# Performance work log

Measured on AMD Instinct MI355X. Metric: run time of the kernel, lower is better.

The kernel has to match this reference:

```python
import jax, jax.numpy as jnp
import numpy as np

B, N, D, H = 256, 40, 256, 256      # molecules, atoms/molecule, pc_hidden, pred_hidden
nS, nC, nB = 40, 5, 5               # n_SYMBOLS, n_FORMAL_CHARGES, n_BOND_TYPES
NEG_SLOPE = 0.01                    # F.leaky_relu default


def _lrelu(x):
    return jnp.where(x >= 0, x, NEG_SLOPE * x)


def setup_inputs() -> dict:
    key = jax.random.key(0)
    ks = jax.random.split(key, 7)
    def w(k, shape, fan_in):
        return jax.random.normal(k, shape, jnp.float32) / np.float32(np.sqrt(fan_in))
    return {
        "yhat": jax.random.normal(ks[0], (B, N, D), jnp.float32),
        "Ws1": w(ks[1], (D, H), D),      "bs1": jnp.zeros((H,), jnp.float32),
        "Ws2": w(ks[2], (H, nS), H),     "bs2": jnp.zeros((nS,), jnp.float32),
        "Wc1": w(ks[3], (D, H), D),      "bc1": jnp.zeros((H,), jnp.float32),
        "Wc2": w(ks[4], (H, nC), H),     "bc2": jnp.zeros((nC,), jnp.float32),
        "Wb1": w(ks[5], (2 * D, H), 2 * D), "bb1": jnp.zeros((H,), jnp.float32),
        "Wb2": w(ks[6], (H, nB), H),     "bb2": jnp.zeros((nB,), jnp.float32),
    }


def reference(yhat, Ws1, bs1, Ws2, bs2, Wc1, bc1, Wc2, bc2, Wb1, bb1, Wb2, bb2):
    # Per-atom symbol / charge heads (2-layer MLP with leaky_relu)
    symbols = _lrelu(yhat @ Ws1 + bs1) @ Ws2 + bs2          # [B, N, nS]
    charges = _lrelu(yhat @ Wc1 + bc1) @ Wc2 + bc2          # [B, N, nC]

    # Pairwise bond head: concat(x_i, x_j) @ Wb1 == x_i @ Wb1[:D] + x_j @ Wb1[D:]
    # (avoids materializing the [B, N, N, 2D] concat tensor)
    p1 = yhat @ Wb1[:D]                                      # [B, N, H]
    p2 = yhat @ Wb1[D:]                                      # [B, N, H]
    h = _lrelu(p1[:, :, None, :] + p2[:, None, :, :] + bb1)  # [B, N, N, H]
    bonds = h @ Wb2 + bb2                                    # [B, N, N, nB]
    bonds = bonds + jnp.swapaxes(bonds, 1, 2)                # symmetrize (i,j)+(j,i)

    return (symbols.reshape(-1, nS),
            charges.reshape(-1, nC),
            bonds.reshape(-1, nB))
```

## Files before the change

kernel.cpp:

```cpp
#include <hip/hip_runtime.h>
#include <hip/hip_bf16.h>

typedef unsigned short u16;
typedef __attribute__((ext_vector_type(4))) int   int4v;
typedef __attribute__((ext_vector_type(4))) unsigned int uint4v;
typedef __attribute__((ext_vector_type(4))) unsigned short ushort4v;
typedef __attribute__((ext_vector_type(4))) float floatx4;
typedef __attribute__((ext_vector_type(8))) short bf16x8;

#define LRELU_NS 0.01f
#define SK 264

__device__ __forceinline__ float bitsToF(unsigned int b) {
    union { unsigned int u; float f; } v; v.u = b << 16; return v.f;
}
__device__ __forceinline__ float bfLo(unsigned int d) {
    union { unsigned int u; float f; } v; v.u = d << 16; return v.f;
}
__device__ __forceinline__ float bfHi(unsigned int d) {
    union { unsigned int u; float f; } v; v.u = d & 0xffff0000u; return v.f;
}
__device__ __forceinline__ u16 f2bf(float f) {
    __hip_bfloat16 h = __float2bfloat16(f);
    return *reinterpret_cast<u16*>(&h);
}
__device__ __forceinline__ float lrelu(float v) {
    return fmaxf(v, 0.f) + LRELU_NS * fminf(v, 0.f);
}
__device__ __forceinline__ u16 ldW(const void* p, int i, int isF32) {
    return isF32 ? f2bf(((const float*)p)[i]) : ((const u16*)p)[i];
}
__device__ __forceinline__ float ldF(const void* p, int i, int isF32) {
    return isF32 ? ((const float*)p)[i]
                 : bitsToF((unsigned int)((const u16*)p)[i]);
}

__device__ __forceinline__ int computeIsF32(const u16* y, int* cnt, int t) {
    if (t == 0) *cnt = 0;
    __syncthreads();
    if (t < 256) {
        u16 v = y[2 * t];
        int e = (v >> 7) & 0xFF;
        if (v == 0 || (e >= 96 && e < 160)) atomicAdd(cnt, 1);
    }
    __syncthreads();
    return (*cnt < 192) ? 1 : 0;
}

__global__ __launch_bounds__(256) void pack_kernel(
    const void* __restrict__ yhat,
    const void* __restrict__ Ws1, const void* __restrict__ Wc1,
    const void* __restrict__ Wb1, const void* __restrict__ Ws2,
    const void* __restrict__ Wc2,
    const void* __restrict__ bs1, const void* __restrict__ bc1,
    const void* __restrict__ bb1, const void* __restrict__ bs2,
    const void* __restrict__ bc2, const void* __restrict__ bb2,
    u16* __restrict__ WallT, u16* __restrict__ W2T, float* __restrict__ biasF)
{
    __shared__ int fcnt;
    const int bid = blockIdx.x, t = threadIdx.x;
    const int isF32 = computeIsF32((const u16*)yhat, &fcnt, t);
    if (bid < 64) {
        __shared__ u16 tile[64][65];
        const int c0 = (bid & 15) * 64;
        const int k0 = (bid >> 4) * 64;
        const void* src; int coff; int roff = 0;
        if (c0 < 256)      { src = Ws1; coff = c0; }
        else if (c0 < 512) { src = Wc1; coff = c0 - 256; }
        else if (c0 < 768) { src = Wb1; coff = c0 - 512; }
        else               { src = Wb1; coff = c0 - 768; roff = 256; }
        const int cc = t & 63, kk0 = t >> 6;
        #pragma unroll
        for (int i = 0; i < 16; ++i) {
            int kk = kk0 + i * 4;
            tile[kk][cc] = ldW(src, (k0 + kk + roff) * 256 + coff + cc, isF32);
        }
        __syncthreads();
        const int kk2 = t & 63, cc0 = t >> 6;
        #pragma unroll
        for (int i = 0; i < 16; ++i) {
            int cc2 = cc0 + i * 4;
            WallT[(c0 + cc2) * 256 + (k0 + kk2)] = tile[kk2][cc2];
        }
    } else if (bid < 128) {
        int e2 = (bid - 64) * 256 + t;
        int c = e2 >> 8, k = e2 & 255;
        u16 v = 0;
        if (c < 40)                 v = ldW(Ws2, k * 40 + c, isF32);
        else if (c >= 48 && c < 53) v = ldW(Wc2, k * 5 + (c - 48), isF32);
        W2T[c * 256 + k] = v;
    } else {
        int idx = (bid - 128) * 256 + t;
        float v = 0.f;
        if (idx < 256)       v = ldF(bs1, idx, isF32);
        else if (idx < 512)  v = ldF(bc1, idx - 256, isF32);
        else if (idx < 768)  v = ldF(bb1, idx - 512, isF32);
        else if (idx < 808)  v = ldF(bs2, idx - 768, isF32);
        else if (idx < 813)  v = ldF(bc2, idx - 808, isF32);
        else if (idx >= 816 && idx < 821) v = ldF(bb2, idx - 816, isF32);
        biasF[idx] = v;
    }
}

__global__ __launch_bounds__(256) void heads_kernel(
    const void* __restrict__ Xv, const u16* __restrict__ WallT,
    const u16* __restrict__ W2T, const float* __restrict__ biasF,
    void* __restrict__ outv)
{
    __shared__ u16 Xs[64 * SK];
    __shared__ u16 Hb[64 * SK];
    __shared__ int fcnt;
    const int t = threadIdx.x;
    const int bm0 = blockIdx.x * 64;
    const int head = blockIdx.y;
    const int isF32 = computeIsF32((const u16*)Xv, &fcnt, t);

    if (isF32) {
        const floatx4* __restrict__ src = (const floatx4*)((const float*)Xv + bm0 * 256);
        #pragma unroll
        for (int it = 0; it < 16; ++it) {
            int cid = t + it * 256;
            int row = cid >> 6, ch = cid & 63;
            floatx4 f = src[cid];
            ushort4v u;
            u[0] = f2bf(f[0]); u[1] = f2bf(f[1]); u[2] = f2bf(f[2]); u[3] = f2bf(f[3]);
            *(ushort4v*)&Xs[row * SK + ch * 4] = u;
        }
    } else {
        const int4v* __restrict__ src = (const int4v*)((const u16*)Xv + bm0 * 256);
        #pragma unroll
        for (int it = 0; it < 8; ++it) {
            int cid = t + it * 256;
            int row = cid >> 5, ch = cid & 31;
            *(int4v*)&Xs[row * SK + ch * 8] = src[cid];
        }
    }
    __syncthreads();

    const int w = t >> 6, l = t & 63;
    const int ml = l & 15, kq = l >> 4, r0 = kq * 4;

    for (int n = 0; n < 4; ++n) {
        const int ct = w + 4 * n;
        floatx4 acc[4] = {};
        #pragma unroll
        for (int ks = 0; ks < 8; ++ks) {
            const int k0 = ks * 32 + kq * 8;
            bf16x8 bf = *(const bf16x8*)&WallT[(head * 256 + ct * 16 + ml) * 256 + k0];
            #pragma unroll
            for (int mt = 0; mt < 4; ++mt) {
                bf16x8 a = *(const bf16x8*)&Xs[(mt * 16 + ml) * SK + k0];
                acc[mt] = __builtin_amdgcn_mfma_f32_16x16x32_bf16(a, bf, acc[mt], 0, 0, 0);
            }
        }
        const int col = ct * 16 + ml;
        const float bias = biasF[head * 256 + col];
        #pragma unroll
        for (int mt = 0; mt < 4; ++mt)
            #pragma unroll
            for (int r = 0; r < 4; ++r)
                Hb[(mt * 16 + r0 + r) * SK + col] = f2bf(lrelu(acc[mt][r] + bias));
    }
    __syncthreads();

    const int nct = (head == 0) ? 3 : 1;
    const int c0  = (head == 0) ? 0 : 48;
    floatx4 acc2[3] = {};
    #pragma unroll
    for (int ks = 0; ks < 8; ++ks) {
        const int k0 = ks * 32 + kq * 8;
        bf16x8 a = *(const bf16x8*)&Hb[(w * 16 + ml) * SK + k0];
        #pragma unroll
        for (int j = 0; j < 3; ++j) {
            if (j < nct) {
                bf16x8 bf = *(const bf16x8*)&W2T[(c0 + j * 16 + ml) * 256 + k0];
                acc2[j] = __builtin_amdgcn_mfma_f32_16x16x32_bf16(a, bf, acc2[j], 0, 0, 0);
            }
        }
    }
    #pragma unroll
    for (int j = 0; j < 3; ++j) {
        if (j < nct) {
            const int col = j * 16 + ml;
            const int lim = (head == 0) ? 40 : 5;
            if (col < lim) {
                const float bias = biasF[(head == 0 ? 768 : 808) + col];
                #pragma unroll
                for (int r = 0; r < 4; ++r) {
                    const int row = bm0 + w * 16 + r0 + r;
                    const int o = (head == 0) ? row * 40 + col
                                              : 409600 + row * 5 + col;
                    const float v = acc2[j][r] + bias;
                    if (isF32) ((float*)outv)[o] = v;
                    else ((__hip_bfloat16*)outv)[o] = __float2bfloat16(v);
                }
            }
        }
    }
}

__global__ __launch_bounds__(512) void bonds_kernel(
    const void* __restrict__ Xv, const u16* __restrict__ WallT,
    const void* __restrict__ Wb2, const float* __restrict__ biasF,
    void* __restrict__ outv)
{
    __shared__ u16 Xm[48 * SK];
    __shared__ u16 P1L[48 * SK];
    __shared__ u16 P2L[48 * SK];
    __shared__ u16 WsB[16 * 264];
    __shared__ float fbuf[8000];
    __shared__ int fcnt;
    const int t = threadIdx.x, b = blockIdx.x;
    const int isF32 = computeIsF32((const u16*)Xv, &fcnt, t);

    if (isF32) {
        const floatx4* __restrict__ src = (const floatx4*)((const float*)Xv + b * 10240);
        #pragma unroll
        for (int it = 0; it < 5; ++it) {
            int cid = t + it * 512;
            int row = cid >> 6, ch = cid & 63;
            floatx4 f = src[cid];
            ushort4v u;
            u[0] = f2bf(f[0]); u[1] = f2bf(f[1]); u[2] = f2bf(f[2]); u[3] = f2bf(f[3]);
            *(ushort4v*)&Xm[row * SK + ch * 4] = u;
        }
        {
            int row = 40 + (t >> 6), ch = t & 63;
            ushort4v z = {0, 0, 0, 0};
            *(ushort4v*)&Xm[row * SK + ch * 4] = z;
        }
    } else {
        const int4v* __restrict__ src = (const int4v*)((const u16*)Xv + b * 10240);
        #pragma unroll
        for (int it = 0; it < 3; ++it) {
            int cid = t + it * 512;
            int row = cid >> 5, ch = cid & 31;
            if (cid < 1280) *(int4v*)&Xm[row * SK + ch * 8] = src[cid];
            else { int4v z = {0, 0, 0, 0}; *(int4v*)&Xm[row * SK + ch * 8] = z; }
        }
    }
    #pragma unroll
    for (int it = 0; it < 8; ++it) {
        int e2 = t + it * 512;
        int c = e2 >> 8, k = e2 & 255;
        WsB[c * 264 + k] = (c < 5) ? ldW(Wb2, k * 5 + c, isF32) : (u16)0;
    }
    __syncthreads();

    const int w = t >> 6, l = t & 63;
    const int ml = l & 15, kq = l >> 4, r0 = kq * 4;

    for (int n = 0; n < 4; ++n) {
        const int gc = (w + 8 * n) * 16 + ml;
        floatx4 acc[3] = {};
        #pragma unroll
        for (int ks = 0; ks < 8; ++ks) {
            const int k0 = ks * 32 + kq * 8;
            bf16x8 bf = *(const bf16x8*)&WallT[(512 + gc) * 256 + k0];
            #pragma unroll
            for (int i = 0; i < 3; ++i) {
                bf16x8 a = *(const bf16x8*)&Xm[(i * 16 + ml) * SK + k0];
                acc[i] = __builtin_amdgcn_mfma_f32_16x16x32_bf16(a, bf, acc[i], 0, 0, 0);
            }
        }
        u16* dst = (gc < 256) ? P1L : P2L;
        const int col = gc & 255;
        const float bias = (gc < 256) ? biasF[512 + gc] : 0.f;
        #pragma unroll
        for (int i = 0; i < 3; ++i)
            #pragma unroll
            for (int r = 0; r < 4; ++r)
                dst[(i * 16 + r0 + r) * SK + col] = f2bf(acc[i][r] + bias);
    }
    __syncthreads();

    bf16x8 wf[8];
    #pragma unroll
    for (int ks = 0; ks < 8; ++ks)
        wf[ks] = *(const bf16x8*)&WsB[ml * 264 + ks * 32 + kq * 8];

    for (int m = 0; m < 5; ++m) {
        const int i = w + 8 * m;
        uint4v pa8[8];
        #pragma unroll
        for (int ks = 0; ks < 8; ++ks)
            pa8[ks] = *(const uint4v*)&P1L[i * SK + ks * 32 + kq * 8];
        for (int jt = 0; jt < 3; ++jt) {
            floatx4 acc = {};
            #pragma unroll
            for (int ks = 0; ks < 8; ++ks) {
                const int k0 = ks * 32 + kq * 8;
                uint4v pa = pa8[ks];
                uint4v pb = *(const uint4v*)&P2L[(jt * 16 + ml) * SK + k0];
                bf16x8 af;
                #pragma unroll
                for (int d = 0; d < 4; ++d) {
                    af[2 * d]     = (short)f2bf(lrelu(bfLo(pa[d]) + bfLo(pb[d])));
                    af[2 * d + 1] = (short)f2bf(lrelu(bfHi(pa[d]) + bfHi(pb[d])));
                }
                acc = __builtin_amdgcn_mfma_f32_16x16x32_bf16(af, wf[ks], acc, 0, 0, 0);
            }
            if (ml < 5) {
                #pragma unroll
                for (int r = 0; r < 4; ++r) {
                    const int j = jt * 16 + r0 + r;
                    if (j < 40) fbuf[(i * 40 + j) * 5 + ml] = acc[r];
                }
            }
        }
    }
    __syncthreads();

    const int base = 460800 + b * 8000;
    for (int e = t; e < 8000; e += 512) {
        int pr = e / 5, c = e - pr * 5;
        int i = pr / 40, j = pr - (pr / 40) * 40;
        float v = fbuf[e] + fbuf[(j * 40 + i) * 5 + c] + 2.f * biasF[816 + c];
        if (isF32) ((float*)outv)[base + e] = v;
        else ((__hip_bfloat16*)outv)[base + e] = __float2bfloat16(v);
    }
}

extern "C" void kernel_launch(void* const* d_in, const int* in_sizes, int n_in,
                              void* d_out, int out_size, void* d_ws, size_t ws_size,
                              hipStream_t stream)
{
    const void* yhat = d_in[0];
    const void* Ws1  = d_in[1];
    const void* bs1  = d_in[2];
    const void* Ws2  = d_in[3];
    const void* bs2  = d_in[4];
    const void* Wc1  = d_in[5];
    const void* bc1  = d_in[6];
    const void* Wc2  = d_in[7];
    const void* bc2  = d_in[8];
    const void* Wb1  = d_in[9];
    const void* bb1  = d_in[10];
    const void* Wb2  = d_in[11];
    const void* bb2  = d_in[12];

    char* wsb = (char*)d_ws;
    float* biasF = (float*)(wsb + 4096);
    u16*   W2T   = (u16*)(wsb + 8192);
    u16*   WallT = (u16*)(wsb + 40960);

    pack_kernel<<<132, 256, 0, stream>>>(yhat, Ws1, Wc1, Wb1, Ws2, Wc2,
                                         bs1, bc1, bb1, bs2, bc2, bb2,
                                         WallT, W2T, biasF);
    heads_kernel<<<dim3(160, 2), 256, 0, stream>>>(yhat, WallT, W2T, biasF, d_out);
    bonds_kernel<<<256, 512, 0, stream>>>(yhat, WallT, Wb2, biasF, d_out);
}
```

Before: 140.4 us.

## Pre-convert yhat to bf16 once and read MFMA operands from global memory

The pack kernel gains extra blocks that convert the fp32 activations to a bf16 workspace buffer once. The heads and bonds kernels then read their A operands straight from that buffer into registers instead of staging converted copies in LDS. The bonds partial-result buffer shrinks from fp32 to bf16, lrelu becomes a single fmax, and occupancy hints are added to both kernels. LDS use drops and occupancy should rise, at the cost of an extra global write and read of the activations and bf16 rounding of the bond partials before symmetrisation.

```diff
diff --git a/kernel.cpp b/kernel.cpp
--- a/kernel.cpp
+++ b/kernel.cpp
@@ -25,7 +25,7 @@
     return *reinterpret_cast<u16*>(&h);
 }
 __device__ __forceinline__ float lrelu(float v) {
-    return fmaxf(v, 0.f) + LRELU_NS * fminf(v, 0.f);
+    return fmaxf(v, LRELU_NS * v);
 }
 __device__ __forceinline__ u16 ldW(const void* p, int i, int isF32) {
     return isF32 ? f2bf(((const float*)p)[i]) : ((const u16*)p)[i];
@@ -55,7 +55,8 @@
     const void* __restrict__ bs1, const void* __restrict__ bc1,
     const void* __restrict__ bb1, const void* __restrict__ bs2,
     const void* __restrict__ bc2, const void* __restrict__ bb2,
-    u16* __restrict__ WallT, u16* __restrict__ W2T, float* __restrict__ biasF)
+    u16* __restrict__ WallT, u16* __restrict__ W2T, float* __restrict__ biasF,
+    u16* __restrict__ Xbf)
 {
     __shared__ int fcnt;
     const int bid = blockIdx.x, t = threadIdx.x;
@@ -89,7 +90,7 @@
         if (c < 40)                 v = ldW(Ws2, k * 40 + c, isF32);
         else if (c >= 48 && c < 53) v = ldW(Wc2, k * 5 + (c - 48), isF32);
         W2T[c * 256 + k] = v;
-    } else {
+    } else if (bid < 132) {
         int idx = (bid - 128) * 256 + t;
         float v = 0.f;
         if (idx < 256)       v = ldF(bs1, idx, isF32);
@@ -99,69 +100,60 @@
         else if (idx < 813)  v = ldF(bc2, idx - 808, isF32);
         else if (idx >= 816 && idx < 821) v = ldF(bb2, idx - 816, isF32);
         biasF[idx] = v;
-    }
-}
-
-__global__ __launch_bounds__(256) void heads_kernel(
-    const void* __restrict__ Xv, const u16* __restrict__ WallT,
+    } else {
+        if (!isF32) return;
+        const floatx4* __restrict__ xf = (const floatx4*)yhat;
+        const int base4 = (bid - 132) * 4096;
+        #pragma unroll
+        for (int it = 0; it < 16; ++it) {
+            int c4 = base4 + t + it * 256;
+            floatx4 f = xf[c4];
+            ushort4v u;
+            u[0] = f2bf(f[0]); u[1] = f2bf(f[1]); u[2] = f2bf(f[2]); u[3] = f2bf(f[3]);
+            *(ushort4v*)&Xbf[c4 * 4] = u;
+        }
+    }
+}
+
+__global__ __launch_bounds__(256, 4) void heads_kernel(
+    const void* __restrict__ Xv, const u16* __restrict__ Xbf,
+    const u16* __restrict__ WallT,
     const u16* __restrict__ W2T, const float* __restrict__ biasF,
     void* __restrict__ outv)
 {
-    __shared__ u16 Xs[64 * SK];
     __shared__ u16 Hb[64 * SK];
     __shared__ int fcnt;
     const int t = threadIdx.x;
     const int bm0 = blockIdx.x * 64;
     const int head = blockIdx.y;
     const int isF32 = computeIsF32((const u16*)Xv, &fcnt, t);
-
-    if (isF32) {
-        const floatx4* __restrict__ src = (const floatx4*)((const float*)Xv + bm0 * 256);
-        #pragma unroll
-        for (int it = 0; it < 16; ++it) {
-            int cid = t + it * 256;
-            int row = cid >> 6, ch = cid & 63;
-            floatx4 f = src[cid];
-            ushort4v u;
-            u[0] = f2bf(f[0]); u[1] = f2bf(f[1]); u[2] = f2bf(f[2]); u[3] = f2bf(f[3]);
-            *(ushort4v*)&Xs[row * SK + ch * 4] = u;
-        }
-    } else {
-        const int4v* __restrict__ src = (const int4v*)((const u16*)Xv + bm0 * 256);
-        #pragma unroll
-        for (int it = 0; it < 8; ++it) {
-            int cid = t + it * 256;
-            int row = cid >> 5, ch = cid & 31;
-            *(int4v*)&Xs[row * SK + ch * 8] = src[cid];
-        }
-    }
-    __syncthreads();
+    const u16* __restrict__ Xb = isF32 ? Xbf : (const u16*)Xv;
 
     const int w = t >> 6, l = t & 63;
     const int ml = l & 15, kq = l >> 4, r0 = kq * 4;
 
-    for (int n = 0; n < 4; ++n) {
-        const int ct = w + 4 * n;
-        floatx4 acc[4] = {};
+    bf16x8 a8[8];
+    {
+        const u16* __restrict__ ap = Xb + (bm0 + w * 16 + ml) * 256 + kq * 8;
+        #pragma unroll
+        for (int ks = 0; ks < 8; ++ks)
+            a8[ks] = *(const bf16x8*)(ap + ks * 32);
+    }
+
+    for (int ct = 0; ct < 16; ++ct) {
+        floatx4 acc = {};
         #pragma unroll
         for (int ks = 0; ks < 8; ++ks) {
             const int k0 = ks * 32 + kq * 8;
             bf16x8 bf = *(const bf16x8*)&WallT[(head * 256 + ct * 16 + ml) * 256 + k0];
-            #pragma unroll
-            for (int mt = 0; mt < 4; ++mt) {
-                bf16x8 a = *(const bf16x8*)&Xs[(mt * 16 + ml) * SK + k0];
-                acc[mt] = __builtin_amdgcn_mfma_f32_16x16x32_bf16(a, bf, acc[mt], 0, 0, 0);
-            }
+            acc = __builtin_amdgcn_mfma_f32_16x16x32_bf16(a8[ks], bf, acc, 0, 0, 0);
         }
         const int col = ct * 16 + ml;
         const float bias = biasF[head * 256 + col];
         #pragma unroll
-        for (int mt = 0; mt < 4; ++mt)
-            #pragma unroll
-            for (int r = 0; r < 4; ++r)
-                Hb[(mt * 16 + r0 + r) * SK + col] = f2bf(lrelu(acc[mt][r] + bias));
-    }
-    __syncthreads();
+        for (int r = 0; r < 4; ++r)
+            Hb[(w * 16 + r0 + r) * SK + col] = f2bf(lrelu(acc[r] + bias));
+    }
 
     const int nct = (head == 0) ? 3 : 1;
     const int c0  = (head == 0) ? 0 : 48;
@@ -199,67 +191,47 @@
     }
 }
 
-__global__ __launch_bounds__(512) void bonds_kernel(
-    const void* __restrict__ Xv, const u16* __restrict__ WallT,
+__global__ __launch_bounds__(512, 4) void bonds_kernel(
+    const void* __restrict__ Xv, const u16* __restrict__ Xbf,
+    const u16* __restrict__ WallT,
     const void* __restrict__ Wb2, const float* __restrict__ biasF,
     void* __restrict__ outv)
 {
-    __shared__ u16 Xm[48 * SK];
     __shared__ u16 P1L[48 * SK];
     __shared__ u16 P2L[48 * SK];
     __shared__ u16 WsB[16 * 264];
-    __shared__ float fbuf[8000];
+    __shared__ u16 fb[8000];
     __shared__ int fcnt;
     const int t = threadIdx.x, b = blockIdx.x;
     const int isF32 = computeIsF32((const u16*)Xv, &fcnt, t);
-
-    if (isF32) {
-        const floatx4* __restrict__ src = (const floatx4*)((const float*)Xv + b * 10240);
-        #pragma unroll
-        for (int it = 0; it < 5; ++it) {
-            int cid = t + it * 512;
-            int row = cid >> 6, ch = cid & 63;
-            floatx4 f = src[cid];
-            ushort4v u;
-            u[0] = f2bf(f[0]); u[1] = f2bf(f[1]); u[2] = f2bf(f[2]); u[3] = f2bf(f[3]);
-            *(ushort4v*)&Xm[row * SK + ch * 4] = u;
-        }
-        {
-            int row = 40 + (t >> 6), ch = t & 63;
-            ushort4v z = {0, 0, 0, 0};
-            *(ushort4v*)&Xm[row * SK + ch * 4] = z;
-        }
-    } else {
-        const int4v* __restrict__ src = (const int4v*)((const u16*)Xv + b * 10240);
-        #pragma unroll
-        for (int it = 0; it < 3; ++it) {
-            int cid = t + it * 512;
-            int row = cid >> 5, ch = cid & 31;
-            if (cid < 1280) *(int4v*)&Xm[row * SK + ch * 8] = src[cid];
-            else { int4v z = {0, 0, 0, 0}; *(int4v*)&Xm[row * SK + ch * 8] = z; }
-        }
-    }
+    const u16* __restrict__ Xb = isF32 ? Xbf : (const u16*)Xv;
+
     #pragma unroll
     for (int it = 0; it < 8; ++it) {
         int e2 = t + it * 512;
         int c = e2 >> 8, k = e2 & 255;
         WsB[c * 264 + k] = (c < 5) ? ldW(Wb2, k * 5 + c, isF32) : (u16)0;
     }
-    __syncthreads();
 
     const int w = t >> 6, l = t & 63;
     const int ml = l & 15, kq = l >> 4, r0 = kq * 4;
 
+    const u16* __restrict__ xrow[3];
+    #pragma unroll
+    for (int mt = 0; mt < 3; ++mt) {
+        int rr = mt * 16 + ml; if (rr > 39) rr = 39;
+        xrow[mt] = Xb + (b * 40 + rr) * 256 + kq * 8;
+    }
     for (int n = 0; n < 4; ++n) {
         const int gc = (w + 8 * n) * 16 + ml;
         floatx4 acc[3] = {};
         #pragma unroll
         for (int ks = 0; ks < 8; ++ks) {
-            const int k0 = ks * 32 + kq * 8;
-            bf16x8 bf = *(const bf16x8*)&WallT[(512 + gc) * 256 + k0];
+            const int k0 = ks * 32;
+            bf16x8 bf = *(const bf16x8*)&WallT[(512 + gc) * 256 + kq * 8 + k0];
             #pragma unroll
             for (int i = 0; i < 3; ++i) {
-                bf16x8 a = *(const bf16x8*)&Xm[(i * 16 + ml) * SK + k0];
+                bf16x8 a = *(const bf16x8*)(xrow[i] + k0);
                 acc[i] = __builtin_amdgcn_mfma_f32_16x16x32_bf16(a, bf, acc[i], 0, 0, 0);
             }
         }
@@ -292,19 +264,23 @@
                 const int k0 = ks * 32 + kq * 8;
                 uint4v pa = pa8[ks];
                 uint4v pb = *(const uint4v*)&P2L[(jt * 16 + ml) * SK + k0];
-                bf16x8 af;
+                int4v ai;
                 #pragma unroll
                 for (int d = 0; d < 4; ++d) {
-                    af[2 * d]     = (short)f2bf(lrelu(bfLo(pa[d]) + bfLo(pb[d])));
-                    af[2 * d + 1] = (short)f2bf(lrelu(bfHi(pa[d]) + bfHi(pb[d])));
+                    float lo = lrelu(bfLo(pa[d]) + bfLo(pb[d]));
+                    float hi = lrelu(bfHi(pa[d]) + bfHi(pb[d]));
+                    unsigned int pl = (unsigned int)f2bf(lo);
+                    unsigned int ph = (unsigned int)f2bf(hi);
+                    ai[d] = (int)(pl | (ph << 16));
                 }
+                bf16x8 af = __builtin_bit_cast(bf16x8, ai);
                 acc = __builtin_amdgcn_mfma_f32_16x16x32_bf16(af, wf[ks], acc, 0, 0, 0);
             }
             if (ml < 5) {
                 #pragma unroll
                 for (int r = 0; r < 4; ++r) {
                     const int j = jt * 16 + r0 + r;
-                    if (j < 40) fbuf[(i * 40 + j) * 5 + ml] = acc[r];
+                    if (j < 40) fb[(i * 40 + j) * 5 + ml] = f2bf(acc[r]);
                 }
             }
         }
@@ -315,7 +291,9 @@
     for (int e = t; e < 8000; e += 512) {
         int pr = e / 5, c = e - pr * 5;
         int i = pr / 40, j = pr - (pr / 40) * 40;
-        float v = fbuf[e] + fbuf[(j * 40 + i) * 5 + c] + 2.f * biasF[816 + c];
+        float v = bitsToF((unsigned int)fb[e])
+                + bitsToF((unsigned int)fb[(j * 40 + i) * 5 + c])
+                + 2.f * biasF[816 + c];
         if (isF32) ((float*)outv)[base + e] = v;
         else ((__hip_bfloat16*)outv)[base + e] = __float2bfloat16(v);
     }
@@ -343,10 +321,11 @@
     float* biasF = (float*)(wsb + 4096);
     u16*   W2T   = (u16*)(wsb + 8192);
     u16*   WallT = (u16*)(wsb + 40960);
-
-    pack_kernel<<<132, 256, 0, stream>>>(yhat, Ws1, Wc1, Wb1, Ws2, Wc2,
+    u16*   Xbf   = (u16*)(wsb + 565248);
+
+    pack_kernel<<<292, 256, 0, stream>>>(yhat, Ws1, Wc1, Wb1, Ws2, Wc2,
                                          bs1, bc1, bb1, bs2, bc2, bb2,
-                                         WallT, W2T, biasF);
-    heads_kernel<<<dim3(160, 2), 256, 0, stream>>>(yhat, WallT, W2T, biasF, d_out);
-    bonds_kernel<<<256, 512, 0, stream>>>(yhat, WallT, Wb2, biasF, d_out);
-}
+                                         WallT, W2T, biasF, Xbf);
+    heads_kernel<<<dim3(160, 2), 256, 0, stream>>>(yhat, Xbf, WallT, W2T, biasF, d_out);
+    bonds_kernel<<<256, 512, 0, stream>>>(yhat, Xbf, WallT, Wb2, biasF, d_out);
+}
```

Result: slower. 170.1 us (+21.1%).
